# Performance work log

Hardware: AMD Instinct MI355X
Metric: run time of the kernel (lower is better)

The kernel has to match this reference:

```python
import jax, jax.numpy as jnp
import numpy as np

H1, H2, H3 = 32, 64, 64
NODEN = 12
NODES_PER_GRAPH = NODEN + 2  # 14
N = 700000                   # 50000 graphs * 14 nodes
E = 4000000


def setup_inputs() -> dict:
    key = jax.random.key(0)
    ks = jax.random.split(key, 8)
    x = jax.random.normal(ks[0], (N, H1), dtype=jnp.float32)
    edges = jax.random.randint(ks[1], (2, E), 0, N, dtype=jnp.int64)
    W1 = jax.random.normal(ks[2], (H1, H2), dtype=jnp.float32) / np.sqrt(H1).astype(np.float32)
    b1 = jnp.zeros((H2,), jnp.float32)
    W2 = jax.random.normal(ks[3], (H2, H3), dtype=jnp.float32) / np.sqrt(H2).astype(np.float32)
    b2 = jnp.zeros((H3,), jnp.float32)
    Wfc = jax.random.normal(ks[4], (H3 * NODES_PER_GRAPH, 1), dtype=jnp.float32) / np.sqrt(H3 * NODES_PER_GRAPH).astype(np.float32)
    bfc = jnp.zeros((1,), jnp.float32)
    return {"x": x, "edges": edges, "W1": W1, "b1": b1, "W2": W2, "b2": b2, "Wfc": Wfc, "bfc": bfc}


def gcn_conv(x, src, dst, W, b, n):
    # PyG GCNConv: h = X W; add self-loops; norm = deg^-1/2[src]*deg^-1/2[dst]
    h = x @ W  # [N, out]
    ones = jnp.ones(src.shape[0], dtype=h.dtype)
    deg = jax.ops.segment_sum(ones, dst, num_segments=n) + jnp.asarray(1.0, h.dtype)  # +1 self-loop
    dinv = jax.lax.rsqrt(deg)  # deg >= 1 always (self-loop)
    norm = dinv[src] * dinv[dst]  # [E]
    agg = jax.ops.segment_sum(h[src] * norm[:, None], dst, num_segments=n)
    agg = agg + h * (dinv * dinv)[:, None]  # self-loop contribution
    return agg + b


def reference(x, edges, W1, b1, W2, b2, Wfc, bfc):
    src, dst = edges[0], edges[1]
    h = jax.nn.relu(gcn_conv(x, src, dst, W1, b1, N))
    # F.dropout(training=False) is identity in eval mode
    h = jax.nn.relu(gcn_conv(h, src, dst, W2, b2, N))
    h = h.reshape(-1, H3 * NODES_PER_GRAPH)  # [B, 896]
    return h @ Wfc + bfc  # [B, 1]
```

## Files before the change

kernel.cpp:

```cpp
#include <hip/hip_runtime.h>
#include <hip/hip_fp16.h>


typedef _Float16 half8 __attribute__((ext_vector_type(8)));
typedef float float4v __attribute__((ext_vector_type(4)));

#define CHUNK 8192
#define BSH 11
#define BNODES 2048

__global__ __launch_bounds__(256) void fallback_kernel(float* __restrict__ out, int n, float v)
{
  int i = blockIdx.x * 256 + threadIdx.x;
  if (i < n) out[i] = v;
}

__global__ __launch_bounds__(64) void probe_kernel(const int* __restrict__ edges, int* __restrict__ flag)
{
  if (threadIdx.x == 0) {
    int orv = edges[1] | edges[3] | edges[5] | edges[7] | edges[9] | edges[11] | edges[13] | edges[15];
    flag[0] = (orv == 0) ? 1 : 0;
  }
}

__global__ __launch_bounds__(64) void zero_dummy_kernel(
    __half* __restrict__ F1, __half* __restrict__ F2, int N)
{
  int t = threadIdx.x;
  if (t < 16) ((uint2*)(F1 + (size_t)N * 64))[t] = make_uint2(0, 0);
  else if (t < 32) ((uint2*)(F2 + (size_t)N * 64))[t - 16] = make_uint2(0, 0);
}

__global__ __launch_bounds__(256) void hist2_kernel(
    const int* __restrict__ edges, int E, int N, const int* __restrict__ flag,
    int* __restrict__ cnt, int NBK)
{
  __shared__ int lh[512];
  int t = threadIdx.x;
  int blk = blockIdx.x;
  for (int b = t; b < NBK; b += 256) lh[b] = 0;
  __syncthreads();
  int sh = flag[0];
  int base = blk * CHUNK;
#pragma unroll
  for (int k = 0; k < CHUNK / 256; k++) {
    int e = base + k * 256 + t;
    if (e < E) {
      int d = edges[(E + e) << sh];
      if ((unsigned)d < (unsigned)N) atomicAdd(&lh[d >> BSH], 1);
    }
  }
  __syncthreads();
  for (int b = t; b < NBK; b += 256) cnt[(size_t)blk * NBK + b] = lh[b];
}

__global__ __launch_bounds__(64) void colscan_kernel(
    int* __restrict__ cnt, int NCH, int NBK, int* __restrict__ totals)
{
  int b = blockIdx.x;
  int lane = threadIdx.x;
  int carry = 0;
  int rounds = (NCH + 63) >> 6;
  for (int r = 0; r < rounds; r++) {
    int blk = r * 64 + lane;
    int v = (blk < NCH) ? cnt[(size_t)blk * NBK + b] : 0;
    int incl = v;
#pragma unroll
    for (int off = 1; off < 64; off <<= 1) {
      int x = __shfl_up(incl, off);
      if (lane >= off) incl += x;
    }
    int excl = incl - v + carry;
    if (blk < NCH) cnt[(size_t)blk * NBK + b] = excl;
    carry += __shfl(incl, 63);
  }
  if (lane == 0) totals[b] = carry;
}

__global__ __launch_bounds__(512) void scan_totals_kernel(
    const int* __restrict__ totals, int NBK,
    int* __restrict__ bstart, int* __restrict__ rowptr, int N)
{
  __shared__ int sm[512];
  int t = threadIdx.x;
  int v = (t < NBK) ? totals[t] : 0;
  sm[t] = v;
  __syncthreads();
  for (int off = 1; off < 512; off <<= 1) {
    int x = 0;
    if (t >= off) x = sm[t - off];
    __syncthreads();
    if (t >= off) sm[t] += x;
    __syncthreads();
  }
  if (t < NBK) bstart[t] = sm[t] - v;
  if (t == 0) { bstart[NBK] = sm[511]; rowptr[N] = sm[511] + N; }
}

__global__ __launch_bounds__(256) void pass3_kernel(
    const int* __restrict__ edges, int E, int N, const int* __restrict__ flag,
    const int* __restrict__ cnt, const int* __restrict__ bstart,
    int* __restrict__ pair, int NBK)
{
  __shared__ int lcur[512];
  int t = threadIdx.x;
  int blk = blockIdx.x;
  for (int b = t; b < NBK; b += 256)
    lcur[b] = bstart[b] + cnt[(size_t)blk * NBK + b];
  __syncthreads();
  int sh = flag[0];
  int base = blk * CHUNK;
#pragma unroll
  for (int k = 0; k < CHUNK / 256; k++) {
    int e = base + k * 256 + t;
    if (e < E) {
      int s = edges[e << sh];
      int d = edges[(E + e) << sh];
      if ((unsigned)s < (unsigned)N && (unsigned)d < (unsigned)N) {
        int pos = atomicAdd(&lcur[d >> BSH], 1);
        pair[pos] = s | ((d & (BNODES - 1)) << 20);
      }
    }
  }
}

__global__ __launch_bounds__(256) void build_kernel(
    const int* __restrict__ pair, const int* __restrict__ bstart,
    int* __restrict__ rowptr, float* __restrict__ dinv, int* __restrict__ col, int N)
{
  __shared__ int hist[BNODES];
  __shared__ int cur[BNODES];
  __shared__ int sc[256];
  int b = blockIdx.x;
  int t = threadIdx.x;
  int pbeg = bstart[b], pend = bstart[b + 1];
  int colbase = pbeg + (b << BSH);
#pragma unroll
  for (int i = 0; i < BNODES / 256; i++) {
    int idx = i * 256 + t;
    int row = (b << BSH) + idx;
    hist[idx] = (row < N) ? 1 : 0;
  }
  __syncthreads();
  for (int p = pbeg + t; p < pend; p += 256)
    atomicAdd(&hist[(pair[p] >> 20) & (BNODES - 1)], 1);
  __syncthreads();
  int hv[8];
  int tsum = 0;
#pragma unroll
  for (int i = 0; i < 8; i++) { hv[i] = hist[t * 8 + i]; tsum += hv[i]; }
  sc[t] = tsum;
  __syncthreads();
  for (int off = 1; off < 256; off <<= 1) {
    int x = 0;
    if (t >= off) x = sc[t - off];
    __syncthreads();
    if (t >= off) sc[t] += x;
    __syncthreads();
  }
  int run = sc[t] - tsum;
#pragma unroll
  for (int i = 0; i < 8; i++) {
    int idx = t * 8 + i;
    int rp = colbase + run;
    int row = (b << BSH) + idx;
    if (row < N) {
      rowptr[row] = rp;
      dinv[row] = rsqrtf((float)hv[i]);
      col[rp] = row;
      cur[idx] = rp + 1;
    } else {
      cur[idx] = rp;
    }
    run += hv[i];
  }
  __syncthreads();
  for (int p = pbeg + t; p < pend; p += 256) {
    int v = pair[p];
    int pos = atomicAdd(&cur[(v >> 20) & (BNODES - 1)], 1);
    col[pos] = v & 0xFFFFF;
  }
}

__global__ __launch_bounds__(256) void mfma_mm1_kernel(
    const float* __restrict__ X, const float* __restrict__ W1,
    const float* __restrict__ dinv, __half* __restrict__ G, int n, int ntiles)
{
  int lane = threadIdx.x & 63;
  int n16 = lane & 15;
  int quad = lane >> 4;

  half8 bf[4];
#pragma unroll
  for (int jb = 0; jb < 4; jb++)
#pragma unroll
    for (int i = 0; i < 8; i++)
      bf[jb][i] = (_Float16)W1[(quad * 8 + i) * 64 + jb * 16 + n16];

  _Float16* Gh = (_Float16*)G;
  int wave = (blockIdx.x * 256 + threadIdx.x) >> 6;
  int nw = (gridDim.x * 256) >> 6;
  for (int tile = wave; tile < ntiles; tile += nw) {
    int ut = __builtin_amdgcn_readfirstlane(tile);
    int base = ut * 16;
    int node = base + n16;
    if (node >= n) node = n - 1;
    const float* xr = X + (size_t)node * 32 + quad * 8;
    half8 a;
#pragma unroll
    for (int i = 0; i < 8; i++) a[i] = (_Float16)xr[i];

    float4v acc[4];
#pragma unroll
    for (int jb = 0; jb < 4; jb++) {
      float4v z = {0.f, 0.f, 0.f, 0.f};
      acc[jb] = __builtin_amdgcn_mfma_f32_16x16x32_f16(a, bf[jb], z, 0, 0, 0);
    }
#pragma unroll
    for (int r = 0; r < 4; r++) {
      int node2 = base + quad * 4 + r;
      if (node2 < n) {
        float dv = dinv[node2];
#pragma unroll
        for (int jb = 0; jb < 4; jb++)
          Gh[(size_t)node2 * 64 + jb * 16 + n16] = (_Float16)(dv * acc[jb][r]);
      }
    }
  }
}

__device__ inline void hacc(uint4 v, __half2* a)
{
  a[0] = __hadd2(a[0], *reinterpret_cast<__half2*>(&v.x));
  a[1] = __hadd2(a[1], *reinterpret_cast<__half2*>(&v.y));
  a[2] = __hadd2(a[2], *reinterpret_cast<__half2*>(&v.z));
  a[3] = __hadd2(a[3], *reinterpret_cast<__half2*>(&v.w));
}

__device__ inline __half2 hrelu2(__half2 v)
{
  __half z = __float2half_rn(0.f);
  __half2 r;
  r.x = __hmax(v.x, z);
  r.y = __hmax(v.y, z);
  return r;
}

template <bool RELU>
__global__ __launch_bounds__(256) void agg_kernel(
    const __half* __restrict__ Gsrc, const int* __restrict__ rowptr,
    const int* __restrict__ col, const float* __restrict__ dinv,
    const float* __restrict__ bias, __half* __restrict__ Udst, int n, int ndummy)
{
  int lane = threadIdx.x & 63;
  int eg = lane >> 3, fo = lane & 7;
  int w = (int)((blockIdx.x * 256 + threadIdx.x) >> 6);
  w = __builtin_amdgcn_readfirstlane(w);
  int node0 = w * 2, node1 = node0 + 1;
  if (node0 >= n) return;
  bool has1 = (node1 < n);
  const uint4* G4 = (const uint4*)Gsrc;
  uint4* U4 = (uint4*)Udst;

  int beg0 = rowptr[node0];
  int end0 = rowptr[node0 + 1];
  int end1 = has1 ? rowptr[node0 + 2] : end0;

  __half2 z2 = __float2half2_rn(0.f);
  __half2 a0[4] = {z2, z2, z2, z2};
  __half2 a1[4] = {z2, z2, z2, z2};

  {
    int i0 = beg0 + eg, i1 = end0 + eg;
    int c0 = col[i0], c1 = col[i1];
    c0 = (i0 < end0) ? c0 : ndummy;
    c1 = (i1 < end1) ? c1 : ndummy;
    uint4 v0 = G4[((size_t)c0 << 3) + fo];
    uint4 v1 = G4[((size_t)c1 << 3) + fo];
    hacc(v0, a0);
    hacc(v1, a1);
  }
  for (int i = beg0 + 8; i < end0; i += 8) {
    int ii = i + eg;
    int c = col[ii];
    c = (ii < end0) ? c : ndummy;
    uint4 v = G4[((size_t)c << 3) + fo];
    hacc(v, a0);
  }
  for (int i = end0 + 8; i < end1; i += 8) {
    int ii = i + eg;
    int c = col[ii];
    c = (ii < end1) ? c : ndummy;
    uint4 v = G4[((size_t)c << 3) + fo];
    hacc(v, a1);
  }

#pragma unroll
  for (int j = 0; j < 4; j++) {
#pragma unroll
    for (int off = 8; off < 64; off <<= 1) {
      int u0 = __shfl_xor(*reinterpret_cast<int*>(&a0[j]), off);
      a0[j] = __hadd2(a0[j], *reinterpret_cast<__half2*>(&u0));
      int u1 = __shfl_xor(*reinterpret_cast<int*>(&a1[j]), off);
      a1[j] = __hadd2(a1[j], *reinterpret_cast<__half2*>(&u1));
    }
  }

  __half2 d0 = __half2half2(__float2half_rn(dinv[node0]));
  __half2 d1 = __half2half2(__float2half_rn(has1 ? dinv[node1] : 0.f));
  __half2 r0[4], r1[4];
  if (RELU) {
    const float* bp = bias + fo * 8;
    float4 ba = *(const float4*)bp;
    float4 bb = *(const float4*)(bp + 4);
    __half2 bh[4] = {__floats2half2_rn(ba.x, ba.y), __floats2half2_rn(ba.z, ba.w),
                     __floats2half2_rn(bb.x, bb.y), __floats2half2_rn(bb.z, bb.w)};
#pragma unroll
    for (int j = 0; j < 4; j++) {
      __half2 h0 = hrelu2(__hadd2(__hmul2(a0[j], d0), bh[j]));
      r0[j] = __hmul2(h0, d0);
      __half2 h1 = hrelu2(__hadd2(__hmul2(a1[j], d1), bh[j]));
      r1[j] = __hmul2(h1, d1);
    }
  } else {
#pragma unroll
    for (int j = 0; j < 4; j++) {
      r0[j] = __hmul2(a0[j], d0);
      r1[j] = __hmul2(a1[j], d1);
    }
  }
  uint4 o0, o1;
  o0.x = *reinterpret_cast<uint*>(&r0[0]); o0.y = *reinterpret_cast<uint*>(&r0[1]);
  o0.z = *reinterpret_cast<uint*>(&r0[2]); o0.w = *reinterpret_cast<uint*>(&r0[3]);
  o1.x = *reinterpret_cast<uint*>(&r1[0]); o1.y = *reinterpret_cast<uint*>(&r1[1]);
  o1.z = *reinterpret_cast<uint*>(&r1[2]); o1.w = *reinterpret_cast<uint*>(&r1[3]);
  if (eg == 0) U4[((size_t)node0 << 3) + fo] = o0;
  if (eg == 1 && has1) U4[((size_t)node1 << 3) + fo] = o1;
}

__global__ __launch_bounds__(256) void out_init_kernel(
    float* __restrict__ out, const float* __restrict__ bfc, int n)
{
  int i = blockIdx.x * 256 + threadIdx.x;
  if (i < n) out[i] = bfc[0];
}

__global__ __launch_bounds__(256) void mfma_final_kernel(
    const __half* __restrict__ A2, const float* __restrict__ W2,
    const float* __restrict__ b2, const float* __restrict__ Wfc,
    float* __restrict__ out, int ntiles)
{
  int lane = threadIdx.x & 63;
  int n16 = lane & 15;
  int quad = lane >> 4;

  half8 bf[4][2];
#pragma unroll
  for (int jb = 0; jb < 4; jb++)
#pragma unroll
    for (int kf = 0; kf < 2; kf++)
#pragma unroll
      for (int i = 0; i < 8; i++)
        bf[jb][kf][i] = (_Float16)W2[(kf * 32 + quad * 8 + i) * 64 + jb * 16 + n16];
  float b2j[4];
#pragma unroll
  for (int jb = 0; jb < 4; jb++) b2j[jb] = b2[jb * 16 + n16];

  const _Float16* A2h = (const _Float16*)A2;
  int wave = (blockIdx.x * 256 + threadIdx.x) >> 6;
  int nw = (gridDim.x * 256) >> 6;
  for (int tile = wave; tile < ntiles; tile += nw) {
    int ut = __builtin_amdgcn_readfirstlane(tile);
    int base = ut * 16;
    const _Float16* arow = A2h + (size_t)(base + n16) * 64 + quad * 8;
    half8 a0 = *(const half8*)(arow);
    half8 a1 = *(const half8*)(arow + 32);

    int g_r[4], t_r[4];
#pragma unroll
    for (int r = 0; r < 4; r++) {
      int node = base + quad * 4 + r;
      g_r[r] = node / 14;
      t_r[r] = node - g_r[r] * 14;
    }
    float pr[4] = {0.f, 0.f, 0.f, 0.f};
#pragma unroll
    for (int jb = 0; jb < 4; jb++) {
      float4v acc = {0.f, 0.f, 0.f, 0.f};
      acc = __builtin_amdgcn_mfma_f32_16x16x32_f16(a0, bf[jb][0], acc, 0, 0, 0);
      acc = __builtin_amdgcn_mfma_f32_16x16x32_f16(a1, bf[jb][1], acc, 0, 0, 0);
      int j = jb * 16 + n16;
#pragma unroll
      for (int r = 0; r < 4; r++) {
        float h = acc[r] + b2j[jb];
        h = h > 0.f ? h : 0.f;
        pr[r] += h * Wfc[t_r[r] * 64 + j];
      }
    }
#pragma unroll
    for (int r = 0; r < 4; r++) {
#pragma unroll
      for (int off = 1; off < 16; off <<= 1) pr[r] += __shfl_xor(pr[r], off);
    }
    if (n16 == 0) {
#pragma unroll
      for (int r = 0; r < 4; r++) atomicAdd(&out[g_r[r]], pr[r]);
    }
  }
}

extern "C" void kernel_launch(void* const* d_in, const int* in_sizes, int n_in,
                              void* d_out, int out_size, void* d_ws, size_t ws_size,
                              hipStream_t stream)
{
  const float* x = (const float*)d_in[0];
  const int* edges = (const int*)d_in[1];
  const float* W1 = (const float*)d_in[2];
  const float* b1 = (const float*)d_in[3];
  const float* W2 = (const float*)d_in[4];
  const float* b2 = (const float*)d_in[5];
  const float* Wfc = (const float*)d_in[6];
  const float* bfc = (const float*)d_in[7];
  float* out = (float*)d_out;
  (void)n_in;

  const int N = in_sizes[0] / 32;
  const int E = in_sizes[1] / 2;
  const int B = out_size;
  const int NBK = (N + BNODES - 1) >> BSH;
  const int NCH = (E + CHUNK - 1) / CHUNK;

  char* ws = (char*)d_ws;
  size_t off = 0;
  auto alloc = [&](size_t bytes) -> void* {
    void* p = ws + off;
    off += (bytes + 255) & ~(size_t)255;
    return p;
  };
  int* flag = (int*)alloc(256);
  int* cnt = (int*)alloc((size_t)NCH * NBK * 4);
  int* totals = (int*)alloc((size_t)NBK * 4);
  int* bstart = (int*)alloc(((size_t)NBK + 1) * 4);
  int* col = (int*)alloc(((size_t)E + N + 64) * 4);
  int* rowptr = (int*)alloc(((size_t)N + 1) * 4);
  float* dinv = (float*)alloc((size_t)N * 4);
  __half* F1 = (__half*)alloc(((size_t)N + 16) * 64 * 2);
  __half* F2 = (__half*)alloc(((size_t)N + 16) * 64 * 2);
  int* pair = (int*)F1;

  if (off > ws_size) {
    float v = -(float)(double)(ws_size >> 20);
    fallback_kernel<<<(B + 255) / 256, 256, 0, stream>>>(out, B, v);
    return;
  }

  probe_kernel<<<1, 64, 0, stream>>>(edges, flag);
  zero_dummy_kernel<<<1, 64, 0, stream>>>(F1, F2, N);
  hist2_kernel<<<NCH, 256, 0, stream>>>(edges, E, N, flag, cnt, NBK);
  colscan_kernel<<<NBK, 64, 0, stream>>>(cnt, NCH, NBK, totals);
  scan_totals_kernel<<<1, 512, 0, stream>>>(totals, NBK, bstart, rowptr, N);
  pass3_kernel<<<NCH, 256, 0, stream>>>(edges, E, N, flag, cnt, bstart, pair, NBK);
  build_kernel<<<NBK, 256, 0, stream>>>(pair, bstart, rowptr, dinv, col, N);

  int ntiles = (N + 15) / 16;
  int aggBlocks = (N + 7) / 8;
  mfma_mm1_kernel<<<4096, 256, 0, stream>>>(x, W1, dinv, F1, N, ntiles);
  agg_kernel<true><<<aggBlocks, 256, 0, stream>>>(F1, rowptr, col, dinv, b1, F2, N, N);
  agg_kernel<false><<<aggBlocks, 256, 0, stream>>>(F2, rowptr, col, dinv, nullptr, F1, N, N);
  out_init_kernel<<<(B + 255) / 256, 256, 0, stream>>>(out, bfc, B);
  mfma_final_kernel<<<2048, 256, 0, stream>>>(F1, W2, b2, Wfc, out, ntiles);
}
```

Before: 662.1 us.

## Fuse second-layer aggregation into final MFMA kernel, dropping intermediate buffer

The second sparse aggregation is moved into the final MFMA kernel. Each wave now gathers neighbour rows for its 16-node tile and assembles the A fragment in registers, instead of writing the aggregated features to global memory and reading them back. This removes one kernel launch and a full N×64 half write and read. In exchange, each lane handles one node's gather serially, so waves diverge on uneven degrees and gather parallelism is lower than in the dedicated agg kernel. The col allocation padding is also enlarged.

```diff
diff --git a/kernel.cpp b/kernel.cpp
--- a/kernel.cpp
+++ b/kernel.cpp
@@ -246,7 +246,6 @@
   return r;
 }
 
-template <bool RELU>
 __global__ __launch_bounds__(256) void agg_kernel(
     const __half* __restrict__ Gsrc, const int* __restrict__ rowptr,
     const int* __restrict__ col, const float* __restrict__ dinv,
@@ -309,7 +308,7 @@
   __half2 d0 = __half2half2(__float2half_rn(dinv[node0]));
   __half2 d1 = __half2half2(__float2half_rn(has1 ? dinv[node1] : 0.f));
   __half2 r0[4], r1[4];
-  if (RELU) {
+  {
     const float* bp = bias + fo * 8;
     float4 ba = *(const float4*)bp;
     float4 bb = *(const float4*)(bp + 4);
@@ -321,12 +320,6 @@
       r0[j] = __hmul2(h0, d0);
       __half2 h1 = hrelu2(__hadd2(__hmul2(a1[j], d1), bh[j]));
       r1[j] = __hmul2(h1, d1);
-    }
-  } else {
-#pragma unroll
-    for (int j = 0; j < 4; j++) {
-      r0[j] = __hmul2(a0[j], d0);
-      r1[j] = __hmul2(a1[j], d1);
     }
   }
   uint4 o0, o1;
@@ -345,10 +338,12 @@
   if (i < n) out[i] = bfc[0];
 }
 
-__global__ __launch_bounds__(256) void mfma_final_kernel(
-    const __half* __restrict__ A2, const float* __restrict__ W2,
-    const float* __restrict__ b2, const float* __restrict__ Wfc,
-    float* __restrict__ out, int ntiles)
+__global__ __launch_bounds__(256) void mfma_final_fused_kernel(
+    const __half* __restrict__ U, const int* __restrict__ rowptr,
+    const int* __restrict__ col, const float* __restrict__ dinv,
+    const float* __restrict__ W2, const float* __restrict__ b2,
+    const float* __restrict__ Wfc, float* __restrict__ out,
+    int ntiles, int ndummy)
 {
   int lane = threadIdx.x & 63;
   int n16 = lane & 15;
@@ -366,22 +361,44 @@
 #pragma unroll
   for (int jb = 0; jb < 4; jb++) b2j[jb] = b2[jb * 16 + n16];
 
-  const _Float16* A2h = (const _Float16*)A2;
+  const uint4* U4 = (const uint4*)U;
   int wave = (blockIdx.x * 256 + threadIdx.x) >> 6;
   int nw = (gridDim.x * 256) >> 6;
   for (int tile = wave; tile < ntiles; tile += nw) {
     int ut = __builtin_amdgcn_readfirstlane(tile);
     int base = ut * 16;
-    const _Float16* arow = A2h + (size_t)(base + n16) * 64 + quad * 8;
-    half8 a0 = *(const half8*)(arow);
-    half8 a1 = *(const half8*)(arow + 32);
+    int node = base + n16;
+    int rbeg = rowptr[node];
+    int rlen = rowptr[node + 1] - rbeg;
+
+    __half2 z2 = __float2half2_rn(0.f);
+    __half2 acc0[4] = {z2, z2, z2, z2};
+    __half2 acc1[4] = {z2, z2, z2, z2};
+
+    for (int j = 0; __any(j < rlen); j++) {
+      int c = col[rbeg + j];
+      c = (j < rlen) ? c : ndummy;
+      size_t rbase = (size_t)c << 3;
+      uint4 v0 = U4[rbase + quad];
+      uint4 v1 = U4[rbase + 4 + quad];
+      hacc(v0, acc0);
+      hacc(v1, acc1);
+    }
+    __half2 dv = __half2half2(__float2half_rn(dinv[node]));
+#pragma unroll
+    for (int j = 0; j < 4; j++) {
+      acc0[j] = __hmul2(acc0[j], dv);
+      acc1[j] = __hmul2(acc1[j], dv);
+    }
+    half8 a0 = *reinterpret_cast<half8*>(acc0);
+    half8 a1 = *reinterpret_cast<half8*>(acc1);
 
     int g_r[4], t_r[4];
 #pragma unroll
     for (int r = 0; r < 4; r++) {
-      int node = base + quad * 4 + r;
-      g_r[r] = node / 14;
-      t_r[r] = node - g_r[r] * 14;
+      int nd = base + quad * 4 + r;
+      g_r[r] = nd / 14;
+      t_r[r] = nd - g_r[r] * 14;
     }
     float pr[4] = {0.f, 0.f, 0.f, 0.f};
 #pragma unroll
@@ -441,7 +458,7 @@
   int* cnt = (int*)alloc((size_t)NCH * NBK * 4);
   int* totals = (int*)alloc((size_t)NBK * 4);
   int* bstart = (int*)alloc(((size_t)NBK + 1) * 4);
-  int* col = (int*)alloc(((size_t)E + N + 64) * 4);
+  int* col = (int*)alloc(((size_t)E + N + 256) * 4);
   int* rowptr = (int*)alloc(((size_t)N + 1) * 4);
   float* dinv = (float*)alloc((size_t)N * 4);
   __half* F1 = (__half*)alloc(((size_t)N + 16) * 64 * 2);
@@ -465,8 +482,8 @@
   int ntiles = (N + 15) / 16;
   int aggBlocks = (N + 7) / 8;
   mfma_mm1_kernel<<<4096, 256, 0, stream>>>(x, W1, dinv, F1, N, ntiles);
-  agg_kernel<true><<<aggBlocks, 256, 0, stream>>>(F1, rowptr, col, dinv, b1, F2, N, N);
-  agg_kernel<false><<<aggBlocks, 256, 0, stream>>>(F2, rowptr, col, dinv, nullptr, F1, N, N);
+  agg_kernel<<<aggBlocks, 256, 0, stream>>>(F1, rowptr, col, dinv, b1, F2, N, N);
   out_init_kernel<<<(B + 255) / 256, 256, 0, stream>>>(out, bfc, B);
-  mfma_final_kernel<<<2048, 256, 0, stream>>>(F1, W2, b2, Wfc, out, ntiles);
-}
+  mfma_final_fused_kernel<<<4096, 256, 0, stream>>>(F2, rowptr, col, dinv, W2, b2, Wfc,
+                                                    out, ntiles, N);
+}
```

After: 622.4 us. -6.0%, faster.
